# Kernel optimization log

Hardware: AMD Instinct MI355X
Metric: run time of the kernel (lower is better)

## Reference

```python
import jax, jax.numpy as jnp
import numpy as np
import math

D_MODEL = 768
H = 12
B = 2
N = 2048


def _layernorm(x, w, b, eps=1e-5):
    mu = jnp.mean(x, axis=-1, keepdims=True)
    var = jnp.var(x, axis=-1, keepdims=True)
    return (x - mu) / jnp.sqrt(var + eps) * w + b


def _mha(q, k, v, h):
    # q,k,v: [B,N,D] -> [B,h,N,dk]
    Bq, Nq, D = q.shape
    dk = D // h
    q = q.reshape(Bq, Nq, h, dk).transpose(0, 2, 1, 3)
    k = k.reshape(Bq, Nq, h, dk).transpose(0, 2, 1, 3)
    v = v.reshape(Bq, Nq, h, dk).transpose(0, 2, 1, 3)
    att = jnp.einsum('bhnd,bhmd->bhnm', q, k) / math.sqrt(dk)
    att = jax.nn.softmax(att, axis=-1)
    out = jnp.einsum('bhnm,bhmd->bhnd', att, v)
    return out.transpose(0, 2, 1, 3).reshape(Bq, Nq, D)


def setup_inputs() -> dict:
    key = jax.random.key(0)
    ks = jax.random.split(key, 12)
    d = D_MODEL
    w = lambda k: jax.random.normal(k, (d, d), jnp.float32) * 0.001
    inp = {
        'rgb': jax.random.normal(ks[0], (B, N, d), jnp.float32),
        'ir': jax.random.normal(ks[1], (B, N, d), jnp.float32),
        'ln0_w': jnp.ones((d,), jnp.float32), 'ln0_b': jnp.zeros((d,), jnp.float32),
        'ln1_w': jnp.ones((d,), jnp.float32), 'ln1_b': jnp.zeros((d,), jnp.float32),
        'Wq_vis': w(ks[2]), 'bq_vis': jnp.zeros((d,), jnp.float32),
        'Wk_vis': w(ks[3]), 'bk_vis': jnp.zeros((d,), jnp.float32),
        'Wq_ir': w(ks[4]), 'bq_ir': jnp.zeros((d,), jnp.float32),
        'Wk_ir': w(ks[5]), 'bk_ir': jnp.zeros((d,), jnp.float32),
        'Wv_vis': w(ks[6]), 'bv_vis': jnp.zeros((d,), jnp.float32),
        'Wv_ir': w(ks[7]), 'bv_ir': jnp.zeros((d,), jnp.float32),
        'Wo_vis': w(ks[8]), 'bo_vis': jnp.zeros((d,), jnp.float32),
        'Wo_ir': w(ks[9]), 'bo_ir': jnp.zeros((d,), jnp.float32),
    }
    return inp


def reference(rgb, ir, ln0_w, ln0_b, ln1_w, ln1_b,
              Wq_vis, bq_vis, Wk_vis, bk_vis, Wq_ir, bq_ir, Wk_ir, bk_ir,
              Wv_vis, bv_vis, Wv_ir, bv_ir, Wo_vis, bo_vis, Wo_ir, bo_ir):
    rgb_n = _layernorm(rgb, ln0_w, ln0_b)
    ir_n = _layernorm(ir, ln1_w, ln1_b)
    q_vis = rgb_n @ Wq_vis + bq_vis
    k_vis = rgb_n @ Wk_vis + bk_vis
    q_ir = ir_n @ Wq_ir + bq_ir
    k_ir = ir_n @ Wk_ir + bk_ir
    v_vis = rgb_n @ Wv_vis + bv_vis
    v_ir = ir_n @ Wv_ir + bv_ir
    out_vis = _mha(q_ir, k_vis, v_vis, H) @ Wo_vis + bo_vis
    out_ir = _mha(q_vis, k_ir, v_ir, H) @ Wo_ir + bo_ir
    return (out_vis, out_ir)
```

## Files before the change

kernel.cpp:

```cpp
#include <hip/hip_runtime.h>
#include <stdint.h>

#define NTOK 4096
#define DM   768

typedef unsigned short u16;
typedef __attribute__((ext_vector_type(8))) short bf16x8;
typedef __attribute__((ext_vector_type(4))) float f32x4;

__device__ __forceinline__ u16 f2bf(float f){
  union { float f; unsigned u; } x; x.f = f;
  return (u16)((x.u + 0x7fffu + ((x.u >> 16) & 1u)) >> 16);
}
__device__ __forceinline__ unsigned fbits(float f){
  union { float f; unsigned u; } x; x.f = f; return x.u;
}

__device__ __forceinline__ void dma16(u16* lds, const u16* g){
  __builtin_amdgcn_global_load_lds(
      (const __attribute__((address_space(1))) unsigned*)g,
      (__attribute__((address_space(3))) unsigned*)lds, 16, 0, 0);
}

struct WcastArgs { const float* src[8]; u16* dst[8]; };

__global__ void k_wcast(WcastArgs a){
  __shared__ float T[64][65];
  int z = blockIdx.z;
  const float* W = a.src[z];
  u16* Wt = a.dst[z];
  int k0 = blockIdx.x * 64, n0 = blockIdx.y * 64;
  int t = threadIdx.x;
  int r = t >> 4, c4 = (t & 15) * 4;
  #pragma unroll
  for (int it = 0; it < 4; ++it){
    int row = r + it * 16;
    float4 v = *(const float4*)(W + (size_t)(k0 + row) * DM + n0 + c4);
    T[row][c4+0] = v.x; T[row][c4+1] = v.y; T[row][c4+2] = v.z; T[row][c4+3] = v.w;
  }
  __syncthreads();
  #pragma unroll
  for (int it = 0; it < 4; ++it){
    int row = r + it * 16;
    union { u16 us[4]; uint2 u2; } pk;
    #pragma unroll
    for (int i = 0; i < 4; i++) pk.us[i] = f2bf(T[c4+i][row]);
    *(uint2*)(Wt + (size_t)(n0 + row) * DM + k0 + c4) = pk.u2;
  }
}

__global__ void k_ln(const float* __restrict__ rgb, const float* __restrict__ ir,
                     const float* __restrict__ w0, const float* __restrict__ b0,
                     const float* __restrict__ w1, const float* __restrict__ b1,
                     u16* __restrict__ rgbn, u16* __restrict__ irn){
  int row = blockIdx.x;
  const float *src, *w, *b; u16* dst;
  if (row < NTOK){ src = rgb + (size_t)row * DM; w = w0; b = b0; dst = rgbn + (size_t)row * DM; }
  else { int r2 = row - NTOK; src = ir + (size_t)r2 * DM; w = w1; b = b1; dst = irn + (size_t)r2 * DM; }
  int t = threadIdx.x;
  float v0 = src[t], v1 = src[t+256], v2 = src[t+512];
  float s = v0+v1+v2, ss = v0*v0 + v1*v1 + v2*v2;
  #pragma unroll
  for (int m = 1; m < 64; m <<= 1){ s += __shfl_xor(s, m, 64); ss += __shfl_xor(ss, m, 64); }
  __shared__ float red[8];
  int wv = t >> 6;
  if ((t & 63) == 0){ red[wv] = s; red[4+wv] = ss; }
  __syncthreads();
  s  = red[0]+red[1]+red[2]+red[3];
  ss = red[4]+red[5]+red[6]+red[7];
  float mu   = s * (1.f/768.f);
  float var  = ss * (1.f/768.f) - mu*mu;
  float rstd = rsqrtf(var + 1e-5f);
  dst[t]     = f2bf((v0-mu)*rstd*w[t]     + b[t]);
  dst[t+256] = f2bf((v1-mu)*rstd*w[t+256] + b[t+256]);
  dst[t+512] = f2bf((v2-mu)*rstd*w[t+512] + b[t+512]);
}

struct GemmArgs { const u16* A[4]; const u16* Bm[4]; const float* bias[4]; void* out[4]; float scale[4]; };

template<int MODE, int NK>
__global__ __launch_bounds__(256) void k_gemm(GemmArgs g){
  __shared__ u16 As[2][128*32];
  __shared__ u16 Bs[2][128*32];
  int z = blockIdx.z;
  const u16* A = g.A[z];
  const u16* B = g.Bm[z];
  const float* bias = g.bias[z];
  float sc = g.scale[z];
  int m0 = blockIdx.x * 128, n0 = blockIdx.y * 128;
  int t = threadIdx.x, lane = t & 63, w = t >> 6, l15 = lane & 15, quad = lane >> 4;
  int wm = (w >> 1) * 64, wn = (w & 1) * 64;
  int lr = lane >> 2, ls = lane & 3;
  int gseg = ls ^ (lr & 3) ^ ((lr >> 2) & 3);
  const u16* Ab = A + (size_t)(m0 + lr) * DM + gseg * 8;
  const u16* Bb = B + (size_t)(n0 + lr) * DM + gseg * 8;
  f32x4 acc[4][4] = {};
  auto stage = [&](int kt, int bufi){
    int k0 = kt * 32;
    #pragma unroll
    for (int c = 0; c < 2; c++){
      int gq = w * 2 + c;
      dma16(&As[bufi][gq*16*32], Ab + (size_t)gq*16*DM + k0);
      dma16(&Bs[bufi][gq*16*32], Bb + (size_t)gq*16*DM + k0);
    }
  };
  stage(0, 0);
  for (int kt = 0; kt < NK; ++kt){
    int cb = kt & 1;
    __syncthreads();
    if (kt + 1 < NK) stage(kt + 1, cb ^ 1);
    bf16x8 af[4], bfr[4];
    #pragma unroll
    for (int i = 0; i < 4; i++){
      int row = wm + i*16 + l15;
      int sg = quad ^ (row & 3) ^ ((row >> 2) & 3);
      af[i] = *(const bf16x8*)&As[cb][row*32 + sg*8];
    }
    #pragma unroll
    for (int j = 0; j < 4; j++){
      int row = wn + j*16 + l15;
      int sg = quad ^ (row & 3) ^ ((row >> 2) & 3);
      bfr[j] = *(const bf16x8*)&Bs[cb][row*32 + sg*8];
    }
    #pragma unroll
    for (int i = 0; i < 4; i++)
      #pragma unroll
      for (int j = 0; j < 4; j++)
        acc[i][j] = __builtin_amdgcn_mfma_f32_16x16x32_bf16(af[i], bfr[j], acc[i][j], 0, 0, 0);
  }
  #pragma unroll
  for (int i = 0; i < 4; i++){
    #pragma unroll
    for (int j = 0; j < 4; j++){
      int col = n0 + wn + j*16 + l15;
      float bc = (MODE == 2) ? 0.f : bias[col];
      #pragma unroll
      for (int r = 0; r < 4; r++){
        int row = m0 + wm + i*16 + quad*4 + r;
        float v;
        if (MODE == 2) v = (acc[i][j][r] + bias[row]) * sc;
        else           v = (acc[i][j][r] + bc) * sc;
        if (MODE == 0)      ((u16*)  g.out[z])[(size_t)row*DM   + col] = f2bf(v);
        else if (MODE == 1) ((float*)g.out[z])[(size_t)row*DM   + col] = v;
        else                ((u16*)  g.out[z])[(size_t)row*4096 + col] = f2bf(v);
      }
    }
  }
}

struct AttnArgs { const u16* q[2]; const u16* k[2]; const u16* vT[2]; u16* o[2]; };

__global__ __launch_bounds__(256, 3) void k_attn(AttnArgs a){
  constexpr int SPP = 72;
  __shared__ u16 Kb[2][64*64];
  __shared__ u16 Vb[2][64*64];
  __shared__ u16 Pb[4][16*SPP];
  int qt = blockIdx.x, bh = blockIdx.y, aid = blockIdx.z;
  int b = bh / 12, h = bh % 12;
  const u16* Q  = a.q[aid]  + (size_t)b*2048*DM + h*64;
  const u16* K  = a.k[aid]  + (size_t)b*2048*DM + h*64;
  const u16* VT = a.vT[aid] + (size_t)h*64*NTOK + (size_t)b*2048;
  u16* O = a.o[aid] + (size_t)b*2048*DM + h*64;
  int t = threadIdx.x, lane = t & 63, w = t >> 6, l15 = lane & 15, quad = lane >> 4;
  bf16x8 aq[2][2];
  #pragma unroll
  for (int i = 0; i < 2; i++)
    #pragma unroll
    for (int hf = 0; hf < 2; hf++)
      aq[i][hf] = *(const bf16x8*)(Q + (size_t)(qt*128 + w*32 + i*16 + l15)*DM + hf*32 + quad*8);
  f32x4 oacc[2][4] = {};
  float psum[2] = {0.f, 0.f};
  int lr = lane >> 3, ls = lane & 7;
  int gsw = ls ^ lr;
  const u16* Kbase = K  + (size_t)lr*DM   + gsw*8;
  const u16* Vbase = VT + (size_t)lr*NTOK + gsw*8;
  auto stage = [&](int kt, int bufi){
    #pragma unroll
    for (int c = 0; c < 2; c++){
      int g = c*4 + w;
      dma16(&Kb[bufi][g*8*64], Kbase + (size_t)(kt*64 + g*8)*DM);
      dma16(&Vb[bufi][g*8*64], Vbase + (size_t)(g*8)*NTOK + kt*64);
    }
  };
  stage(0, 0);
  u16* Pw = &Pb[w][0];
  for (int kt = 0; kt < 32; ++kt){
    int cb = kt & 1;
    __syncthreads();
    if (kt < 31) stage(kt + 1, cb ^ 1);
    bf16x8 kf[4][2], vf[4][2];
    #pragma unroll
    for (int j = 0; j < 4; j++){
      int row = j*16 + l15, sw = row & 7;
      #pragma unroll
      for (int hf = 0; hf < 2; hf++){
        kf[j][hf] = *(const bf16x8*)&Kb[cb][row*64 + ((hf*4 + quad) ^ sw)*8];
        vf[j][hf] = *(const bf16x8*)&Vb[cb][row*64 + ((hf*4 + quad) ^ sw)*8];
      }
    }
    #pragma unroll
    for (int i = 0; i < 2; i++){
      f32x4 st[4];
      #pragma unroll
      for (int j = 0; j < 4; j++){
        f32x4 s = {0.f, 0.f, 0.f, 0.f};
        s = __builtin_amdgcn_mfma_f32_16x16x32_bf16(kf[j][0], aq[i][0], s, 0, 0, 0);
        s = __builtin_amdgcn_mfma_f32_16x16x32_bf16(kf[j][1], aq[i][1], s, 0, 0, 0);
        st[j] = s;
      }
      #pragma unroll
      for (int j = 0; j < 4; j++){
        float p0 = __builtin_amdgcn_exp2f(st[j][0]);
        float p1 = __builtin_amdgcn_exp2f(st[j][1]);
        float p2 = __builtin_amdgcn_exp2f(st[j][2]);
        float p3 = __builtin_amdgcn_exp2f(st[j][3]);
        psum[i] += (p0 + p1) + (p2 + p3);
        uint2 pk;
        pk.x = __builtin_amdgcn_perm(fbits(p1), fbits(p0), 0x07060302u);
        pk.y = __builtin_amdgcn_perm(fbits(p3), fbits(p2), 0x07060302u);
        *(uint2*)&Pw[l15*SPP + j*16 + quad*4] = pk;
      }
      #pragma unroll
      for (int s2 = 0; s2 < 2; s2++){
        bf16x8 ap = *(const bf16x8*)&Pw[l15*SPP + s2*32 + quad*8];
        #pragma unroll
        for (int j = 0; j < 4; j++)
          oacc[i][j] = __builtin_amdgcn_mfma_f32_16x16x32_bf16(ap, vf[j][s2], oacc[i][j], 0, 0, 0);
      }
    }
  }
  #pragma unroll
  for (int i = 0; i < 2; i++){
    float s = psum[i];
    s += __shfl_xor(s, 16, 64);
    s += __shfl_xor(s, 32, 64);
    float invs = 1.f / s;
    float oinv[4];
    #pragma unroll
    for (int r = 0; r < 4; r++) oinv[r] = __shfl(invs, quad*4 + r, 64);
    #pragma unroll
    for (int j = 0; j < 4; j++)
      #pragma unroll
      for (int r = 0; r < 4; r++){
        int row = qt*128 + w*32 + i*16 + quad*4 + r;
        O[(size_t)row*DM + j*16 + l15] = f2bf(oacc[i][j][r] * oinv[r]);
      }
  }
}

extern "C" void kernel_launch(void* const* d_in, const int* in_sizes, int n_in,
                              void* d_out, int out_size, void* d_ws, size_t ws_size,
                              hipStream_t stream){
  const float* rgb  = (const float*)d_in[0];
  const float* ir   = (const float*)d_in[1];
  const float* ln0w = (const float*)d_in[2];
  const float* ln0b = (const float*)d_in[3];
  const float* ln1w = (const float*)d_in[4];
  const float* ln1b = (const float*)d_in[5];
  const float* Wq_vis = (const float*)d_in[6];  const float* bq_vis = (const float*)d_in[7];
  const float* Wk_vis = (const float*)d_in[8];  const float* bk_vis = (const float*)d_in[9];
  const float* Wq_ir  = (const float*)d_in[10]; const float* bq_ir  = (const float*)d_in[11];
  const float* Wk_ir  = (const float*)d_in[12]; const float* bk_ir  = (const float*)d_in[13];
  const float* Wv_vis = (const float*)d_in[14]; const float* bv_vis = (const float*)d_in[15];
  const float* Wv_ir  = (const float*)d_in[16]; const float* bv_ir  = (const float*)d_in[17];
  const float* Wo_vis = (const float*)d_in[18]; const float* bo_vis = (const float*)d_in[19];
  const float* Wo_ir  = (const float*)d_in[20]; const float* bo_ir  = (const float*)d_in[21];
  float* out = (float*)d_out;

  char* ws = (char*)d_ws;
  size_t off = 0;
  auto alloc = [&](size_t bytes)->void*{
    void* p = ws + off; off += (bytes + 255) & ~(size_t)255; return p;
  };
  const size_t MAT = (size_t)NTOK * DM;
  u16* Wt[8];
  for (int i = 0; i < 8; i++) Wt[i] = (u16*)alloc((size_t)DM * DM * 2);
  u16* rgbn = (u16*)alloc(MAT*2);
  u16* irn  = (u16*)alloc(MAT*2);
  u16* qv = (u16*)alloc(MAT*2); u16* kv = (u16*)alloc(MAT*2);
  u16* qi = (u16*)alloc(MAT*2); u16* ki = (u16*)alloc(MAT*2);
  u16* tv  = (u16*)alloc(MAT*2);
  u16* ti  = (u16*)alloc(MAT*2);
  u16* at0 = (u16*)alloc(MAT*2);
  u16* at1 = (u16*)alloc(MAT*2);

  WcastArgs wa;
  const float* wsrc[8] = {Wq_vis, Wk_vis, Wv_vis, Wq_ir, Wk_ir, Wv_ir, Wo_vis, Wo_ir};
  for (int i = 0; i < 8; i++){ wa.src[i] = wsrc[i]; wa.dst[i] = Wt[i]; }
  k_wcast<<<dim3(12,12,8), 256, 0, stream>>>(wa);

  k_ln<<<dim3(2*NTOK), 256, 0, stream>>>(rgb, ir, ln0w, ln0b, ln1w, ln1b, rgbn, irn);

  const float QS = 0.125f * 1.44269504088896f;
  GemmArgs gp = {};
  gp.A[0]=rgbn; gp.Bm[0]=Wt[0]; gp.bias[0]=bq_vis; gp.out[0]=qv; gp.scale[0]=QS;
  gp.A[1]=rgbn; gp.Bm[1]=Wt[1]; gp.bias[1]=bk_vis; gp.out[1]=kv; gp.scale[1]=1.f;
  gp.A[2]=irn;  gp.Bm[2]=Wt[3]; gp.bias[2]=bq_ir;  gp.out[2]=qi; gp.scale[2]=QS;
  gp.A[3]=irn;  gp.Bm[3]=Wt[4]; gp.bias[3]=bk_ir;  gp.out[3]=ki; gp.scale[3]=1.f;
  k_gemm<0,24><<<dim3(32,6,4), 256, 0, stream>>>(gp);

  GemmArgs gv = {};
  gv.A[0]=Wt[2]; gv.Bm[0]=rgbn; gv.bias[0]=bv_vis; gv.out[0]=tv; gv.scale[0]=1.f;
  gv.A[1]=Wt[5]; gv.Bm[1]=irn;  gv.bias[1]=bv_ir;  gv.out[1]=ti; gv.scale[1]=1.f;
  k_gemm<2,24><<<dim3(6,32,2), 256, 0, stream>>>(gv);

  AttnArgs aa;
  aa.q[0]=qi; aa.k[0]=kv; aa.vT[0]=tv; aa.o[0]=at0;
  aa.q[1]=qv; aa.k[1]=ki; aa.vT[1]=ti; aa.o[1]=at1;
  k_attn<<<dim3(16,24,2), 256, 0, stream>>>(aa);

  GemmArgs gf = {};
  gf.A[0]=at0; gf.Bm[0]=Wt[6]; gf.bias[0]=bo_vis; gf.out[0]=out;       gf.scale[0]=1.f;
  gf.A[1]=at1; gf.Bm[1]=Wt[7]; gf.bias[1]=bo_ir;  gf.out[1]=out + MAT; gf.scale[1]=1.f;
  k_gemm<1,24><<<dim3(32,6,2), 256, 0, stream>>>(gf);
}
```

Measured before the change: 274.8 us.

## Keep attention probabilities in registers via permuted V layout and merge launches

The V-transpose GEMM now writes its output with a column permutation. This lets the attention kernel feed the exp'd score accumulators directly as the MFMA B operand, so the per-wave LDS staging buffer for P is no longer needed. Without that buffer, occupancy is raised to 4 blocks per SM, and the output store becomes a packed 8-byte write per token. Separately, the weight cast and layernorm are merged into one launch, and the QK and V projections share a single runtime-mode GEMM launch, which cuts kernel count at the cost of runtime mode branches.

```diff
diff --git a/kernel.cpp b/kernel.cpp
--- a/kernel.cpp
+++ b/kernel.cpp
@@ -14,6 +14,9 @@
 }
 __device__ __forceinline__ unsigned fbits(float f){
   union { float f; unsigned u; } x; x.f = f; return x.u;
+}
+__device__ __forceinline__ int invk(int t){
+  return (((t>>3)&1)<<4) | (((t>>2)&1)<<3) | (((t>>4)&1)<<2) | (t&3);
 }
 
 __device__ __forceinline__ void dma16(u16* lds, const u16* g){
@@ -22,72 +25,77 @@
       (__attribute__((address_space(3))) unsigned*)lds, 16, 0, 0);
 }
 
-struct WcastArgs { const float* src[8]; u16* dst[8]; };
-
-__global__ void k_wcast(WcastArgs a){
+struct PreArgs {
+  const float* wsrc[8]; u16* wdst[8];
+  const float* rgb; const float* ir;
+  const float* w0; const float* b0; const float* w1; const float* b1;
+  u16* rgbn; u16* irn;
+};
+
+__global__ __launch_bounds__(256) void k_pre(PreArgs a){
   __shared__ float T[64][65];
-  int z = blockIdx.z;
-  const float* W = a.src[z];
-  u16* Wt = a.dst[z];
-  int k0 = blockIdx.x * 64, n0 = blockIdx.y * 64;
+  __shared__ float red[8];
+  int bid = blockIdx.x;
   int t = threadIdx.x;
-  int r = t >> 4, c4 = (t & 15) * 4;
-  #pragma unroll
-  for (int it = 0; it < 4; ++it){
-    int row = r + it * 16;
-    float4 v = *(const float4*)(W + (size_t)(k0 + row) * DM + n0 + c4);
-    T[row][c4+0] = v.x; T[row][c4+1] = v.y; T[row][c4+2] = v.z; T[row][c4+3] = v.w;
-  }
-  __syncthreads();
-  #pragma unroll
-  for (int it = 0; it < 4; ++it){
-    int row = r + it * 16;
-    union { u16 us[4]; uint2 u2; } pk;
-    #pragma unroll
-    for (int i = 0; i < 4; i++) pk.us[i] = f2bf(T[c4+i][row]);
-    *(uint2*)(Wt + (size_t)(n0 + row) * DM + k0 + c4) = pk.u2;
-  }
-}
-
-__global__ void k_ln(const float* __restrict__ rgb, const float* __restrict__ ir,
-                     const float* __restrict__ w0, const float* __restrict__ b0,
-                     const float* __restrict__ w1, const float* __restrict__ b1,
-                     u16* __restrict__ rgbn, u16* __restrict__ irn){
-  int row = blockIdx.x;
-  const float *src, *w, *b; u16* dst;
-  if (row < NTOK){ src = rgb + (size_t)row * DM; w = w0; b = b0; dst = rgbn + (size_t)row * DM; }
-  else { int r2 = row - NTOK; src = ir + (size_t)r2 * DM; w = w1; b = b1; dst = irn + (size_t)r2 * DM; }
-  int t = threadIdx.x;
-  float v0 = src[t], v1 = src[t+256], v2 = src[t+512];
-  float s = v0+v1+v2, ss = v0*v0 + v1*v1 + v2*v2;
-  #pragma unroll
-  for (int m = 1; m < 64; m <<= 1){ s += __shfl_xor(s, m, 64); ss += __shfl_xor(ss, m, 64); }
-  __shared__ float red[8];
-  int wv = t >> 6;
-  if ((t & 63) == 0){ red[wv] = s; red[4+wv] = ss; }
-  __syncthreads();
-  s  = red[0]+red[1]+red[2]+red[3];
-  ss = red[4]+red[5]+red[6]+red[7];
-  float mu   = s * (1.f/768.f);
-  float var  = ss * (1.f/768.f) - mu*mu;
-  float rstd = rsqrtf(var + 1e-5f);
-  dst[t]     = f2bf((v0-mu)*rstd*w[t]     + b[t]);
-  dst[t+256] = f2bf((v1-mu)*rstd*w[t+256] + b[t+256]);
-  dst[t+512] = f2bf((v2-mu)*rstd*w[t+512] + b[t+512]);
-}
-
-struct GemmArgs { const u16* A[4]; const u16* Bm[4]; const float* bias[4]; void* out[4]; float scale[4]; };
-
-template<int MODE, int NK>
-__global__ __launch_bounds__(256) void k_gemm(GemmArgs g){
+  if (bid < 1152){
+    int z = bid / 144, r = bid % 144;
+    int k0 = (r % 12) * 64, n0 = (r / 12) * 64;
+    const float* W = a.wsrc[z];
+    u16* Wt = a.wdst[z];
+    int rr = t >> 4, c4 = (t & 15) * 4;
+    #pragma unroll
+    for (int it = 0; it < 4; ++it){
+      int row = rr + it * 16;
+      float4 v = *(const float4*)(W + (size_t)(k0 + row) * DM + n0 + c4);
+      T[row][c4+0] = v.x; T[row][c4+1] = v.y; T[row][c4+2] = v.z; T[row][c4+3] = v.w;
+    }
+    __syncthreads();
+    #pragma unroll
+    for (int it = 0; it < 4; ++it){
+      int row = rr + it * 16;
+      union { u16 us[4]; uint2 u2; } pk;
+      #pragma unroll
+      for (int i = 0; i < 4; i++) pk.us[i] = f2bf(T[c4+i][row]);
+      *(uint2*)(Wt + (size_t)(n0 + row) * DM + k0 + c4) = pk.u2;
+    }
+  } else {
+    int row = bid - 1152;
+    const float *src, *w, *b; u16* dst;
+    if (row < NTOK){ src = a.rgb + (size_t)row * DM; w = a.w0; b = a.b0; dst = a.rgbn + (size_t)row * DM; }
+    else { int r2 = row - NTOK; src = a.ir + (size_t)r2 * DM; w = a.w1; b = a.b1; dst = a.irn + (size_t)r2 * DM; }
+    float v0 = src[t], v1 = src[t+256], v2 = src[t+512];
+    float s = v0+v1+v2, ss = v0*v0 + v1*v1 + v2*v2;
+    #pragma unroll
+    for (int m = 1; m < 64; m <<= 1){ s += __shfl_xor(s, m, 64); ss += __shfl_xor(ss, m, 64); }
+    int wv = t >> 6;
+    if ((t & 63) == 0){ red[wv] = s; red[4+wv] = ss; }
+    __syncthreads();
+    s  = red[0]+red[1]+red[2]+red[3];
+    ss = red[4]+red[5]+red[6]+red[7];
+    float mu   = s * (1.f/768.f);
+    float var  = ss * (1.f/768.f) - mu*mu;
+    float rstd = rsqrtf(var + 1e-5f);
+    dst[t]     = f2bf((v0-mu)*rstd*w[t]     + b[t]);
+    dst[t+256] = f2bf((v1-mu)*rstd*w[t+256] + b[t+256]);
+    dst[t+512] = f2bf((v2-mu)*rstd*w[t+512] + b[t+512]);
+  }
+}
+
+struct MmArgs { const u16* A[6]; const u16* Bm[6]; const float* bias[6]; void* out[6]; float scale[6]; int mode[6]; };
+
+__global__ __launch_bounds__(256) void k_mm(MmArgs g){
   __shared__ u16 As[2][128*32];
   __shared__ u16 Bs[2][128*32];
   int z = blockIdx.z;
+  int mode = g.mode[z];
   const u16* A = g.A[z];
   const u16* B = g.Bm[z];
   const float* bias = g.bias[z];
   float sc = g.scale[z];
-  int m0 = blockIdx.x * 128, n0 = blockIdx.y * 128;
+  int bx = blockIdx.x;
+  int m0, n0;
+  if (mode == 2){ m0 = (bx % 6) * 128; n0 = (bx / 6) * 128; }
+  else          { m0 = (bx & 31) * 128; n0 = (bx >> 5) * 128; }
   int t = threadIdx.x, lane = t & 63, w = t >> 6, l15 = lane & 15, quad = lane >> 4;
   int wm = (w >> 1) * 64, wn = (w & 1) * 64;
   int lr = lane >> 2, ls = lane & 3;
@@ -105,10 +113,10 @@
     }
   };
   stage(0, 0);
-  for (int kt = 0; kt < NK; ++kt){
+  for (int kt = 0; kt < 24; ++kt){
     int cb = kt & 1;
     __syncthreads();
-    if (kt + 1 < NK) stage(kt + 1, cb ^ 1);
+    if (kt + 1 < 24) stage(kt + 1, cb ^ 1);
     bf16x8 af[4], bfr[4];
     #pragma unroll
     for (int i = 0; i < 4; i++){
@@ -128,33 +136,42 @@
       for (int j = 0; j < 4; j++)
         acc[i][j] = __builtin_amdgcn_mfma_f32_16x16x32_bf16(af[i], bfr[j], acc[i][j], 0, 0, 0);
   }
-  #pragma unroll
-  for (int i = 0; i < 4; i++){
-    #pragma unroll
-    for (int j = 0; j < 4; j++){
-      int col = n0 + wn + j*16 + l15;
-      float bc = (MODE == 2) ? 0.f : bias[col];
-      #pragma unroll
-      for (int r = 0; r < 4; r++){
-        int row = m0 + wm + i*16 + quad*4 + r;
-        float v;
-        if (MODE == 2) v = (acc[i][j][r] + bias[row]) * sc;
-        else           v = (acc[i][j][r] + bc) * sc;
-        if (MODE == 0)      ((u16*)  g.out[z])[(size_t)row*DM   + col] = f2bf(v);
-        else if (MODE == 1) ((float*)g.out[z])[(size_t)row*DM   + col] = v;
-        else                ((u16*)  g.out[z])[(size_t)row*4096 + col] = f2bf(v);
-      }
-    }
+  if (mode == 2){
+    #pragma unroll
+    for (int i = 0; i < 4; i++)
+      #pragma unroll
+      for (int j = 0; j < 4; j++){
+        int colt = n0 + wn + j*16 + l15;
+        int pc = (colt & ~31) | invk(colt & 31);
+        #pragma unroll
+        for (int r = 0; r < 4; r++){
+          int row = m0 + wm + i*16 + quad*4 + r;
+          ((u16*)g.out[z])[(size_t)row*4096 + pc] = f2bf((acc[i][j][r] + bias[row]) * sc);
+        }
+      }
+  } else {
+    #pragma unroll
+    for (int i = 0; i < 4; i++)
+      #pragma unroll
+      for (int j = 0; j < 4; j++){
+        int col = n0 + wn + j*16 + l15;
+        float bc = bias[col];
+        #pragma unroll
+        for (int r = 0; r < 4; r++){
+          int row = m0 + wm + i*16 + quad*4 + r;
+          float v = (acc[i][j][r] + bc) * sc;
+          if (mode == 1) ((float*)g.out[z])[(size_t)row*DM + col] = v;
+          else           ((u16*) g.out[z])[(size_t)row*DM + col] = f2bf(v);
+        }
+      }
   }
 }
 
 struct AttnArgs { const u16* q[2]; const u16* k[2]; const u16* vT[2]; u16* o[2]; };
 
-__global__ __launch_bounds__(256, 3) void k_attn(AttnArgs a){
-  constexpr int SPP = 72;
+__global__ __launch_bounds__(256, 4) void k_attn(AttnArgs a){
   __shared__ u16 Kb[2][64*64];
   __shared__ u16 Vb[2][64*64];
-  __shared__ u16 Pb[4][16*SPP];
   int qt = blockIdx.x, bh = blockIdx.y, aid = blockIdx.z;
   int b = bh / 12, h = bh % 12;
   const u16* Q  = a.q[aid]  + (size_t)b*2048*DM + h*64;
@@ -183,7 +200,6 @@
     }
   };
   stage(0, 0);
-  u16* Pw = &Pb[w][0];
   for (int kt = 0; kt < 32; ++kt){
     int cb = kt & 1;
     __syncthreads();
@@ -208,24 +224,23 @@
         s = __builtin_amdgcn_mfma_f32_16x16x32_bf16(kf[j][1], aq[i][1], s, 0, 0, 0);
         st[j] = s;
       }
+      f32x4 pe[4];
       #pragma unroll
       for (int j = 0; j < 4; j++){
-        float p0 = __builtin_amdgcn_exp2f(st[j][0]);
-        float p1 = __builtin_amdgcn_exp2f(st[j][1]);
-        float p2 = __builtin_amdgcn_exp2f(st[j][2]);
-        float p3 = __builtin_amdgcn_exp2f(st[j][3]);
-        psum[i] += (p0 + p1) + (p2 + p3);
-        uint2 pk;
-        pk.x = __builtin_amdgcn_perm(fbits(p1), fbits(p0), 0x07060302u);
-        pk.y = __builtin_amdgcn_perm(fbits(p3), fbits(p2), 0x07060302u);
-        *(uint2*)&Pw[l15*SPP + j*16 + quad*4] = pk;
-      }
-      #pragma unroll
-      for (int s2 = 0; s2 < 2; s2++){
-        bf16x8 ap = *(const bf16x8*)&Pw[l15*SPP + s2*32 + quad*8];
+        #pragma unroll
+        for (int r = 0; r < 4; r++) pe[j][r] = __builtin_amdgcn_exp2f(st[j][r]);
+        psum[i] += (pe[j][0] + pe[j][1]) + (pe[j][2] + pe[j][3]);
+      }
+      #pragma unroll
+      for (int h2 = 0; h2 < 2; h2++){
+        union { uint4 u; bf16x8 v; } pf;
+        pf.u.x = __builtin_amdgcn_perm(fbits(pe[2*h2][1]),   fbits(pe[2*h2][0]),   0x07060302u);
+        pf.u.y = __builtin_amdgcn_perm(fbits(pe[2*h2][3]),   fbits(pe[2*h2][2]),   0x07060302u);
+        pf.u.z = __builtin_amdgcn_perm(fbits(pe[2*h2+1][1]), fbits(pe[2*h2+1][0]), 0x07060302u);
+        pf.u.w = __builtin_amdgcn_perm(fbits(pe[2*h2+1][3]), fbits(pe[2*h2+1][2]), 0x07060302u);
         #pragma unroll
         for (int j = 0; j < 4; j++)
-          oacc[i][j] = __builtin_amdgcn_mfma_f32_16x16x32_bf16(ap, vf[j][s2], oacc[i][j], 0, 0, 0);
+          oacc[i][j] = __builtin_amdgcn_mfma_f32_16x16x32_bf16(vf[j][h2], pf.v, oacc[i][j], 0, 0, 0);
       }
     }
   }
@@ -234,17 +249,17 @@
     float s = psum[i];
     s += __shfl_xor(s, 16, 64);
     s += __shfl_xor(s, 32, 64);
-    float invs = 1.f / s;
-    float oinv[4];
-    #pragma unroll
-    for (int r = 0; r < 4; r++) oinv[r] = __shfl(invs, quad*4 + r, 64);
-    #pragma unroll
-    for (int j = 0; j < 4; j++)
-      #pragma unroll
-      for (int r = 0; r < 4; r++){
-        int row = qt*128 + w*32 + i*16 + quad*4 + r;
-        O[(size_t)row*DM + j*16 + l15] = f2bf(oacc[i][j][r] * oinv[r]);
-      }
+    float oinv = 1.f / s;
+    int token = qt*128 + w*32 + i*16 + l15;
+    #pragma unroll
+    for (int j = 0; j < 4; j++){
+      float v0 = oacc[i][j][0] * oinv, v1 = oacc[i][j][1] * oinv;
+      float v2 = oacc[i][j][2] * oinv, v3 = oacc[i][j][3] * oinv;
+      uint2 pk;
+      pk.x = (unsigned)f2bf(v0) | ((unsigned)f2bf(v1) << 16);
+      pk.y = (unsigned)f2bf(v2) | ((unsigned)f2bf(v3) << 16);
+      *(uint2*)&O[(size_t)token*DM + j*16 + quad*4] = pk;
+    }
   }
 }
 
@@ -284,33 +299,30 @@
   u16* at0 = (u16*)alloc(MAT*2);
   u16* at1 = (u16*)alloc(MAT*2);
 
-  WcastArgs wa;
+  PreArgs pa;
   const float* wsrc[8] = {Wq_vis, Wk_vis, Wv_vis, Wq_ir, Wk_ir, Wv_ir, Wo_vis, Wo_ir};
-  for (int i = 0; i < 8; i++){ wa.src[i] = wsrc[i]; wa.dst[i] = Wt[i]; }
-  k_wcast<<<dim3(12,12,8), 256, 0, stream>>>(wa);
-
-  k_ln<<<dim3(2*NTOK), 256, 0, stream>>>(rgb, ir, ln0w, ln0b, ln1w, ln1b, rgbn, irn);
+  for (int i = 0; i < 8; i++){ pa.wsrc[i] = wsrc[i]; pa.wdst[i] = Wt[i]; }
+  pa.rgb = rgb; pa.ir = ir; pa.w0 = ln0w; pa.b0 = ln0b; pa.w1 = ln1w; pa.b1 = ln1b;
+  pa.rgbn = rgbn; pa.irn = irn;
+  k_pre<<<dim3(1152 + 2*NTOK), 256, 0, stream>>>(pa);
 
   const float QS = 0.125f * 1.44269504088896f;
-  GemmArgs gp = {};
-  gp.A[0]=rgbn; gp.Bm[0]=Wt[0]; gp.bias[0]=bq_vis; gp.out[0]=qv; gp.scale[0]=QS;
-  gp.A[1]=rgbn; gp.Bm[1]=Wt[1]; gp.bias[1]=bk_vis; gp.out[1]=kv; gp.scale[1]=1.f;
-  gp.A[2]=irn;  gp.Bm[2]=Wt[3]; gp.bias[2]=bq_ir;  gp.out[2]=qi; gp.scale[2]=QS;
-  gp.A[3]=irn;  gp.Bm[3]=Wt[4]; gp.bias[3]=bk_ir;  gp.out[3]=ki; gp.scale[3]=1.f;
-  k_gemm<0,24><<<dim3(32,6,4), 256, 0, stream>>>(gp);
-
-  GemmArgs gv = {};
-  gv.A[0]=Wt[2]; gv.Bm[0]=rgbn; gv.bias[0]=bv_vis; gv.out[0]=tv; gv.scale[0]=1.f;
-  gv.A[1]=Wt[5]; gv.Bm[1]=irn;  gv.bias[1]=bv_ir;  gv.out[1]=ti; gv.scale[1]=1.f;
-  k_gemm<2,24><<<dim3(6,32,2), 256, 0, stream>>>(gv);
+  MmArgs gp = {};
+  gp.A[0]=rgbn; gp.Bm[0]=Wt[0]; gp.bias[0]=bq_vis; gp.out[0]=qv; gp.scale[0]=QS;  gp.mode[0]=0;
+  gp.A[1]=rgbn; gp.Bm[1]=Wt[1]; gp.bias[1]=bk_vis; gp.out[1]=kv; gp.scale[1]=1.f; gp.mode[1]=0;
+  gp.A[2]=irn;  gp.Bm[2]=Wt[3]; gp.bias[2]=bq_ir;  gp.out[2]=qi; gp.scale[2]=QS;  gp.mode[2]=0;
+  gp.A[3]=irn;  gp.Bm[3]=Wt[4]; gp.bias[3]=bk_ir;  gp.out[3]=ki; gp.scale[3]=1.f; gp.mode[3]=0;
+  gp.A[4]=Wt[2]; gp.Bm[4]=rgbn; gp.bias[4]=bv_vis; gp.out[4]=tv; gp.scale[4]=1.f; gp.mode[4]=2;
+  gp.A[5]=Wt[5]; gp.Bm[5]=irn;  gp.bias[5]=bv_ir;  gp.out[5]=ti; gp.scale[5]=1.f; gp.mode[5]=2;
+  k_mm<<<dim3(192,1,6), 256, 0, stream>>>(gp);
 
   AttnArgs aa;
   aa.q[0]=qi; aa.k[0]=kv; aa.vT[0]=tv; aa.o[0]=at0;
   aa.q[1]=qv; aa.k[1]=ki; aa.vT[1]=ti; aa.o[1]=at1;
   k_attn<<<dim3(16,24,2), 256, 0, stream>>>(aa);
 
-  GemmArgs gf = {};
-  gf.A[0]=at0; gf.Bm[0]=Wt[6]; gf.bias[0]=bo_vis; gf.out[0]=out;       gf.scale[0]=1.f;
-  gf.A[1]=at1; gf.Bm[1]=Wt[7]; gf.bias[1]=bo_ir;  gf.out[1]=out + MAT; gf.scale[1]=1.f;
-  k_gemm<1,24><<<dim3(32,6,2), 256, 0, stream>>>(gf);
-}
+  MmArgs gf = {};
+  gf.A[0]=at0; gf.Bm[0]=Wt[6]; gf.bias[0]=bo_vis; gf.out[0]=out;       gf.scale[0]=1.f; gf.mode[0]=1;
+  gf.A[1]=at1; gf.Bm[1]=Wt[7]; gf.bias[1]=bo_ir;  gf.out[1]=out + MAT; gf.scale[1]=1.f; gf.mode[1]=1;
+  k_mm<<<dim3(192,1,2), 256, 0, stream>>>(gf);
+}
```

Result: faster. 266.0 us (-3.2%).
